# Optimization experiments

Hardware: AMD Instinct MI355X
Metric: run time of the kernel (lower is better)

The kernel has to match this reference:

```python
import jax, jax.numpy as jnp
import numpy as np

B, T, C, H, D = 2048, 64, 64, 8, 64  # batch, block_size, n_embed, num_heads, head_size


def setup_inputs() -> dict:
    key = jax.random.key(0)
    ks = jax.random.split(key, 6)
    s = C ** -0.5  # approx torch Linear init scale
    x = jax.random.normal(ks[0], (B, T, C), dtype=jnp.float32)
    Wq = jax.random.uniform(ks[1], (H, C, D), jnp.float32, -s, s)  # per-head query weights (in, out)
    Wk = jax.random.uniform(ks[2], (H, C, D), jnp.float32, -s, s)
    Wv = jax.random.uniform(ks[3], (H, C, D), jnp.float32, -s, s)
    sp = (H * D) ** -0.5
    Wproj = jax.random.uniform(ks[4], (H * D, C), jnp.float32, -sp, sp)  # proj weight (in, out)
    bproj = jax.random.uniform(ks[5], (C,), jnp.float32, -sp, sp)
    return {"x": x, "Wq": Wq, "Wk": Wk, "Wv": Wv, "Wproj": Wproj, "bproj": bproj}


def reference(x, Wq, Wk, Wv, Wproj, bproj):
    # per-head projections, vectorized over heads (original loops over Head modules)
    q = jnp.einsum('btc,hcd->bhtd', x, Wq)
    k = jnp.einsum('btc,hcd->bhtd', x, Wk)
    v = jnp.einsum('btc,hcd->bhtd', x, Wv)
    scores = jnp.einsum('bhtd,bhsd->bhts', q, k) * (D ** -0.5)  # [B,H,T,T]
    causal = jnp.tril(jnp.ones((T, T), dtype=bool))
    scores = jnp.where(causal, scores, jnp.float32(-jnp.inf))
    wei = jax.nn.softmax(scores, axis=-1)  # dropout = identity in eval mode
    out = jnp.einsum('bhts,bhsd->bhtd', wei, v)
    out = out.transpose(0, 2, 1, 3).reshape(B, T, H * D)  # concat heads on last dim
    out = out @ Wproj + bproj  # output projection (dropout = identity in eval)
    return out
```

## Files before the change

kernel.cpp:

```cpp
#include <hip/hip_runtime.h>

typedef __bf16 bf16x8 __attribute__((ext_vector_type(8)));
typedef float f32x4 __attribute__((ext_vector_type(4)));
typedef unsigned short u16x4 __attribute__((ext_vector_type(4)));
typedef unsigned int u32x4 __attribute__((ext_vector_type(4)));

#define LDA 72

template <int N> struct Int { static constexpr int value = N; };

__device__ __forceinline__ unsigned short f2bf(float f) {
  __bf16 b = (__bf16)f;
  return __builtin_bit_cast(unsigned short, b);
}

__device__ __forceinline__ u16x4 pack4(f32x4 v) {
  u16x4 r;
  r[0] = f2bf(v[0]); r[1] = f2bf(v[1]); r[2] = f2bf(v[2]); r[3] = f2bf(v[3]);
  return r;
}

__device__ __forceinline__ bf16x8 frag8(const unsigned short* p) {
  typedef unsigned short u16x8v __attribute__((ext_vector_type(8)));
  return __builtin_bit_cast(bf16x8, *reinterpret_cast<const u16x8v*>(p));
}

#define MFMA(a, b, c) __builtin_amdgcn_mfma_f32_16x16x32_bf16(a, b, c, 0, 0, 0)

__device__ __forceinline__ void cfrag2bfrag(const f32x4 v[4], bf16x8 out[2]) {
  unsigned O[4][2];
  #pragma unroll
  for (int si = 0; si < 4; ++si) {
    u16x4 p = pack4(v[si]);
    O[si][0] = (unsigned)p[0] | ((unsigned)p[1] << 16);
    O[si][1] = (unsigned)p[2] | ((unsigned)p[3] << 16);
  }
  unsigned H[2][2][2];
  #pragma unroll
  for (int s1 = 0; s1 < 2; ++s1)
    #pragma unroll
    for (int d = 0; d < 2; ++d) {
      auto r = __builtin_amdgcn_permlane32_swap(O[2 * s1][d], O[2 * s1 + 1][d], false, false);
      H[s1][0][d] = r[0];
      H[s1][1][d] = r[1];
    }
  #pragma unroll
  for (int e1 = 0; e1 < 2; ++e1) {
    auto r0 = __builtin_amdgcn_permlane16_swap(H[e1][0][0], H[e1][1][0], false, false);
    auto r1 = __builtin_amdgcn_permlane16_swap(H[e1][0][1], H[e1][1][1], false, false);
    u32x4 f;
    f[0] = r0[0]; f[1] = r1[0]; f[2] = r0[1]; f[3] = r1[1];
    out[e1] = __builtin_bit_cast(bf16x8, f);
  }
}

__global__ __launch_bounds__(256) void fuse_pack(
    const float* __restrict__ Wq, const float* __restrict__ Wk,
    const float* __restrict__ Wv, const float* __restrict__ Wp,
    unsigned short* __restrict__ wf) {
  __shared__ float A[64 * 65];
  __shared__ float B[64 * 65];
  const int blk = blockIdx.x;
  const int t = blk >> 3, h = blk & 7;
  const int tid = threadIdx.x;
  const float* Asrc = (t ? Wv : Wq) + h * 4096;
  const float* Bsrc = (t ? Wp : Wk) + h * 4096;
  for (int i = tid; i < 4096; i += 256) {
    A[(i >> 6) * 65 + (i & 63)] = Asrc[i];
    B[(i >> 6) * 65 + (i & 63)] = Bsrc[i];
  }
  __syncthreads();
  unsigned short* dst = wf + blk * 4096;
  for (int o = 0; o < 16; ++o) {
    int idx = o * 256 + tid;
    int k = idx >> 6, n = idx & 63;
    float s = 0.f;
    if (t == 0) {
      for (int d = 0; d < 64; ++d) s += A[k * 65 + d] * B[n * 65 + d];
      s *= 0.18033688f;
    } else {
      for (int d = 0; d < 64; ++d) s += A[k * 65 + d] * B[d * 65 + n];
    }
    int kk = k >> 5, i = k & 7, lg = (k >> 3) & 3, si = n >> 4, l15 = n & 15;
    dst[((kk * 4 + si) * 64 + lg * 16 + l15) * 8 + i] = f2bf(s);
  }
}

__global__ __launch_bounds__(256, 4) void mha_fwd(
    const float* __restrict__ x, const unsigned short* __restrict__ wf,
    const float* __restrict__ bproj, float* __restrict__ out) {
  __shared__ __attribute__((aligned(16))) unsigned short Xs[2][64 * LDA];

  const int tid  = threadIdx.x;
  const int lane = tid & 63;
  const int w    = tid >> 6;
  const int bt   = w >> 1;
  const int mg   = w & 1;
  const int l15  = lane & 15;
  const int g    = lane >> 4;
  const int kcol = 8 * g;

  const float* xb = x + (size_t)blockIdx.x * 8192;
  #pragma unroll
  for (int it = 0; it < 8; ++it) {
    int idx = it * 1024 + tid * 4;
    float4 v = *reinterpret_cast<const float4*>(xb + idx);
    f32x4 vv = {v.x, v.y, v.z, v.w};
    int sb = idx >> 12, rem = idx & 4095;
    *reinterpret_cast<u16x4*>(&Xs[sb][(rem >> 6) * LDA + (rem & 63)]) = pack4(vv);
  }
  __syncthreads();

  bf16x8 xf[2][4];
  #pragma unroll
  for (int cc = 0; cc < 2; ++cc)
    #pragma unroll
    for (int t = 0; t < 4; ++t)
      xf[cc][t] = frag8(&Xs[bt][(t * 16 + l15) * LDA + cc * 32 + kcol]);

  f32x4 oacc[2][4];
  #pragma unroll
  for (int nt = 0; nt < 4; ++nt) {
    float bias = bproj[nt * 16 + l15];
    f32x4 bv = {bias, bias, bias, bias};
    oacc[0][nt] = bv;
    oacc[1][nt] = bv;
  }

  #pragma unroll 1
  for (int h = 0; h < 8; ++h) {
    const unsigned short* mf = wf + h * 4096;
    const unsigned short* nf = wf + 32768 + h * 4096;

    auto head_body = [&](auto MT0C, auto MT1C) {
      constexpr int MT0 = decltype(MT0C)::value;
      constexpr int MT1 = decltype(MT1C)::value;
      bf16x8 pA[2][2];

      auto gs = [&](auto MTC, int lmt) {
        constexpr int MT = decltype(MTC)::value;
        f32x4 gc[4] = {};
        #pragma unroll
        for (int kk = 0; kk < 2; ++kk)
          #pragma unroll
          for (int ct = 0; ct < 4; ++ct)
            gc[ct] = MFMA(frag8(&mf[(kk * 4 + ct) * 512 + lane * 8]), xf[kk][MT], gc[ct]);
        bf16x8 gB[2];
        cfrag2bfrag(gc, gB);

        f32x4 sc[4] = {};
        #pragma unroll
        for (int cc = 0; cc < 2; ++cc)
          #pragma unroll
          for (int st = 0; st < 4; ++st)
            if (st <= MT)
              sc[st] = MFMA(xf[cc][st], gB[cc], sc[st]);

        const int m = MT * 16 + l15;
        float sum = 0.f;
        #pragma unroll
        for (int st = 0; st < 4; ++st) {
          if (st < MT) {
            #pragma unroll
            for (int r = 0; r < 4; ++r) { float e = exp2f(sc[st][r]); sc[st][r] = e; sum += e; }
          } else if (st == MT) {
            #pragma unroll
            for (int r = 0; r < 4; ++r) {
              int s = st * 16 + 4 * g + r;
              float e = (s <= m) ? exp2f(sc[st][r]) : 0.f;
              sc[st][r] = e; sum += e;
            }
          }
        }
        sum += __shfl_xor(sum, 16);
        sum += __shfl_xor(sum, 32);
        float rinv = __builtin_amdgcn_rcpf(sum);
        #pragma unroll
        for (int st = 0; st < 4; ++st)
          if (st <= MT) sc[st] *= rinv;
        bf16x8 o2[2];
        cfrag2bfrag(sc, o2);
        pA[0][lmt] = o2[0]; pA[1][lmt] = o2[1];
      };
      gs(Int<MT0>{}, 0);
      gs(Int<MT1>{}, 1);

      #pragma unroll
      for (int nt = 0; nt < 4; ++nt) {
        bf16x8 nf0 = frag8(&nf[nt * 512 + lane * 8]);
        bf16x8 nf1 = frag8(&nf[(4 + nt) * 512 + lane * 8]);
        f32x4 zc[4] = {};
        #pragma unroll
        for (int st = 0; st < 4; ++st) {
          zc[st] = MFMA(xf[0][st], nf0, zc[st]);
          zc[st] = MFMA(xf[1][st], nf1, zc[st]);
        }
        bf16x8 zB[2];
        cfrag2bfrag(zc, zB);
        oacc[0][nt] = MFMA(pA[0][0], zB[0], oacc[0][nt]);
        if (MT0 >= 2) oacc[0][nt] = MFMA(pA[1][0], zB[1], oacc[0][nt]);
        oacc[1][nt] = MFMA(pA[0][1], zB[0], oacc[1][nt]);
        if (MT1 >= 2) oacc[1][nt] = MFMA(pA[1][1], zB[1], oacc[1][nt]);
      }
    };

    if (mg == 0) head_body(Int<0>{}, Int<3>{});
    else         head_body(Int<1>{}, Int<2>{});
  }

  const int mtv0 = mg ? 1 : 0;
  const int mtv1 = mg ? 2 : 3;
  float* ob = out + ((size_t)blockIdx.x * 2 + bt) * 4096;
  #pragma unroll
  for (int lmt = 0; lmt < 2; ++lmt) {
    int mt = lmt ? mtv1 : mtv0;
    #pragma unroll
    for (int r = 0; r < 4; ++r) {
      float* orow = ob + (mt * 16 + 4 * g + r) * 64;
      #pragma unroll
      for (int nt = 0; nt < 4; ++nt)
        orow[nt * 16 + l15] = oacc[lmt][nt][r];
    }
  }
}

extern "C" void kernel_launch(void* const* d_in, const int* in_sizes, int n_in,
                              void* d_out, int out_size, void* d_ws, size_t ws_size,
                              hipStream_t stream) {
  const float* x  = (const float*)d_in[0];
  const float* Wq = (const float*)d_in[1];
  const float* Wk = (const float*)d_in[2];
  const float* Wv = (const float*)d_in[3];
  const float* Wp = (const float*)d_in[4];
  const float* bp = (const float*)d_in[5];
  unsigned short* wf = (unsigned short*)d_ws;

  fuse_pack<<<dim3(16), dim3(256), 0, stream>>>(Wq, Wk, Wv, Wp, wf);
  mha_fwd<<<dim3(1024), dim3(256), 0, stream>>>(x, wf, bp, (float*)d_out);
}
```

Measured before the change: 61.28 us.

## Reassociate output path to compute (P·X)·Wvp instead of P·(X·Wvp)

The value/output path is reordered. The attention probabilities are first multiplied with a transposed bf16 copy of X kept in shared memory, and the result is then multiplied by the fused Wv·Wproj weights, instead of projecting all of X per head and then applying P. This cuts the MFMA count per head and the number of fragment layout conversions, and it uses the causal structure of each row tile. The cost is a second transposed LDS buffer, which doubles shared memory per block and can limit occupancy. It also adds scalar 16-bit transposed stores during staging, which may hit bank conflicts, and the fused weight fragments are reloaded once per row tile.

```diff
diff --git a/kernel.cpp b/kernel.cpp
--- a/kernel.cpp
+++ b/kernel.cpp
@@ -90,6 +90,7 @@
     const float* __restrict__ x, const unsigned short* __restrict__ wf,
     const float* __restrict__ bproj, float* __restrict__ out) {
   __shared__ __attribute__((aligned(16))) unsigned short Xs[2][64 * LDA];
+  __shared__ __attribute__((aligned(16))) unsigned short XsT[2][64 * LDA];
 
   const int tid  = threadIdx.x;
   const int lane = tid & 63;
@@ -107,7 +108,12 @@
     float4 v = *reinterpret_cast<const float4*>(xb + idx);
     f32x4 vv = {v.x, v.y, v.z, v.w};
     int sb = idx >> 12, rem = idx & 4095;
-    *reinterpret_cast<u16x4*>(&Xs[sb][(rem >> 6) * LDA + (rem & 63)]) = pack4(vv);
+    int r = rem >> 6, c0 = rem & 63;
+    u16x4 pk = pack4(vv);
+    *reinterpret_cast<u16x4*>(&Xs[sb][r * LDA + c0]) = pk;
+    #pragma unroll
+    for (int j = 0; j < 4; ++j)
+      XsT[sb][(c0 + j) * LDA + r] = pk[j];
   }
   __syncthreads();
 
@@ -185,23 +191,28 @@
       gs(Int<MT0>{}, 0);
       gs(Int<MT1>{}, 1);
 
-      #pragma unroll
-      for (int nt = 0; nt < 4; ++nt) {
-        bf16x8 nf0 = frag8(&nf[nt * 512 + lane * 8]);
-        bf16x8 nf1 = frag8(&nf[(4 + nt) * 512 + lane * 8]);
-        f32x4 zc[4] = {};
-        #pragma unroll
-        for (int st = 0; st < 4; ++st) {
-          zc[st] = MFMA(xf[0][st], nf0, zc[st]);
-          zc[st] = MFMA(xf[1][st], nf1, zc[st]);
+      auto ypv = [&](auto MTC, int lmt) {
+        constexpr int MT = decltype(MTC)::value;
+        f32x4 ytc[4] = {};
+        #pragma unroll
+        for (int ct = 0; ct < 4; ++ct) {
+          bf16x8 xb0 = frag8(&XsT[bt][(ct * 16 + l15) * LDA + kcol]);
+          ytc[ct] = MFMA(xb0, pA[0][lmt], ytc[ct]);
+          if (MT >= 2) {
+            bf16x8 xb1 = frag8(&XsT[bt][(ct * 16 + l15) * LDA + 32 + kcol]);
+            ytc[ct] = MFMA(xb1, pA[1][lmt], ytc[ct]);
+          }
         }
-        bf16x8 zB[2];
-        cfrag2bfrag(zc, zB);
-        oacc[0][nt] = MFMA(pA[0][0], zB[0], oacc[0][nt]);
-        if (MT0 >= 2) oacc[0][nt] = MFMA(pA[1][0], zB[1], oacc[0][nt]);
-        oacc[1][nt] = MFMA(pA[0][1], zB[0], oacc[1][nt]);
-        if (MT1 >= 2) oacc[1][nt] = MFMA(pA[1][1], zB[1], oacc[1][nt]);
-      }
+        bf16x8 yA[2];
+        cfrag2bfrag(ytc, yA);
+        #pragma unroll
+        for (int nt = 0; nt < 4; ++nt) {
+          oacc[lmt][nt] = MFMA(yA[0], frag8(&nf[nt * 512 + lane * 8]), oacc[lmt][nt]);
+          oacc[lmt][nt] = MFMA(yA[1], frag8(&nf[(4 + nt) * 512 + lane * 8]), oacc[lmt][nt]);
+        }
+      };
+      ypv(Int<MT0>{}, 0);
+      ypv(Int<MT1>{}, 1);
     };
 
     if (mg == 0) head_body(Int<0>{}, Int<3>{});
```

New measurement: 63.84 us. 1.04x slower.

## Split per-head Z projection across wave pair and share via LDS

Applied to the files above, without the earlier changes.

Before, both waves covering the same batch element computed the full x·(Wv·Wproj) product for every head, so that work was done twice. Now each wave computes half of the output column tiles, writes the bf16 fragments to shared memory, and after a barrier both waves read the full set. This halves the Z-projection MFMA work in exchange for LDS traffic and one block-wide barrier per head. The Z buffers are double-buffered by head parity, and the shared memory holding the staged x is reused for them after an extra barrier.

```diff
diff --git a/kernel.cpp b/kernel.cpp
--- a/kernel.cpp
+++ b/kernel.cpp
@@ -3,6 +3,7 @@
 typedef __bf16 bf16x8 __attribute__((ext_vector_type(8)));
 typedef float f32x4 __attribute__((ext_vector_type(4)));
 typedef unsigned short u16x4 __attribute__((ext_vector_type(4)));
+typedef unsigned short u16x8 __attribute__((ext_vector_type(8)));
 typedef unsigned int u32x4 __attribute__((ext_vector_type(4)));
 
 #define LDA 72
@@ -21,8 +22,7 @@
 }
 
 __device__ __forceinline__ bf16x8 frag8(const unsigned short* p) {
-  typedef unsigned short u16x8v __attribute__((ext_vector_type(8)));
-  return __builtin_bit_cast(bf16x8, *reinterpret_cast<const u16x8v*>(p));
+  return __builtin_bit_cast(bf16x8, *reinterpret_cast<const u16x8*>(p));
 }
 
 #define MFMA(a, b, c) __builtin_amdgcn_mfma_f32_16x16x32_bf16(a, b, c, 0, 0, 0)
@@ -89,7 +89,9 @@
 __global__ __launch_bounds__(256, 4) void mha_fwd(
     const float* __restrict__ x, const unsigned short* __restrict__ wf,
     const float* __restrict__ bproj, float* __restrict__ out) {
-  __shared__ __attribute__((aligned(16))) unsigned short Xs[2][64 * LDA];
+  __shared__ __attribute__((aligned(16))) unsigned char smem[32768];
+  unsigned short* XsBase = reinterpret_cast<unsigned short*>(smem);
+  unsigned short* ZsBase = reinterpret_cast<unsigned short*>(smem);
 
   const int tid  = threadIdx.x;
   const int lane = tid & 63;
@@ -107,7 +109,7 @@
     float4 v = *reinterpret_cast<const float4*>(xb + idx);
     f32x4 vv = {v.x, v.y, v.z, v.w};
     int sb = idx >> 12, rem = idx & 4095;
-    *reinterpret_cast<u16x4*>(&Xs[sb][(rem >> 6) * LDA + (rem & 63)]) = pack4(vv);
+    *reinterpret_cast<u16x4*>(&XsBase[sb * (64 * LDA) + (rem >> 6) * LDA + (rem & 63)]) = pack4(vv);
   }
   __syncthreads();
 
@@ -116,7 +118,8 @@
   for (int cc = 0; cc < 2; ++cc)
     #pragma unroll
     for (int t = 0; t < 4; ++t)
-      xf[cc][t] = frag8(&Xs[bt][(t * 16 + l15) * LDA + cc * 32 + kcol]);
+      xf[cc][t] = frag8(&XsBase[bt * (64 * LDA) + (t * 16 + l15) * LDA + cc * 32 + kcol]);
+  __syncthreads();
 
   f32x4 oacc[2][4];
   #pragma unroll
@@ -131,12 +134,32 @@
   for (int h = 0; h < 8; ++h) {
     const unsigned short* mf = wf + h * 4096;
     const unsigned short* nf = wf + 32768 + h * 4096;
+    unsigned short* zs = ZsBase + ((bt * 2 + (h & 1)) * 8) * 64 * 8;
 
     auto head_body = [&](auto MT0C, auto MT1C) {
       constexpr int MT0 = decltype(MT0C)::value;
       constexpr int MT1 = decltype(MT1C)::value;
+
+      #pragma unroll
+      for (int l = 0; l < 2; ++l) {
+        const int ntg = 2 * mg + l;
+        bf16x8 nf0 = frag8(&nf[ntg * 512 + lane * 8]);
+        bf16x8 nf1 = frag8(&nf[(4 + ntg) * 512 + lane * 8]);
+        f32x4 zc[4] = {};
+        #pragma unroll
+        for (int st = 0; st < 4; ++st) {
+          zc[st] = MFMA(xf[0][st], nf0, zc[st]);
+          zc[st] = MFMA(xf[1][st], nf1, zc[st]);
+        }
+        bf16x8 zb[2];
+        cfrag2bfrag(zc, zb);
+        #pragma unroll
+        for (int cc = 0; cc < 2; ++cc)
+          *reinterpret_cast<u16x8*>(&zs[((ntg * 2 + cc) * 64 + lane) * 8]) =
+              __builtin_bit_cast(u16x8, zb[cc]);
+      }
+
       bf16x8 pA[2][2];
-
       auto gs = [&](auto MTC, int lmt) {
         constexpr int MT = decltype(MTC)::value;
         f32x4 gc[4] = {};
@@ -185,22 +208,16 @@
       gs(Int<MT0>{}, 0);
       gs(Int<MT1>{}, 1);
 
+      __syncthreads();
+
       #pragma unroll
       for (int nt = 0; nt < 4; ++nt) {
-        bf16x8 nf0 = frag8(&nf[nt * 512 + lane * 8]);
-        bf16x8 nf1 = frag8(&nf[(4 + nt) * 512 + lane * 8]);
-        f32x4 zc[4] = {};
-        #pragma unroll
-        for (int st = 0; st < 4; ++st) {
-          zc[st] = MFMA(xf[0][st], nf0, zc[st]);
-          zc[st] = MFMA(xf[1][st], nf1, zc[st]);
-        }
-        bf16x8 zB[2];
-        cfrag2bfrag(zc, zB);
-        oacc[0][nt] = MFMA(pA[0][0], zB[0], oacc[0][nt]);
-        if (MT0 >= 2) oacc[0][nt] = MFMA(pA[1][0], zB[1], oacc[0][nt]);
-        oacc[1][nt] = MFMA(pA[0][1], zB[0], oacc[1][nt]);
-        if (MT1 >= 2) oacc[1][nt] = MFMA(pA[1][1], zB[1], oacc[1][nt]);
+        bf16x8 zb0 = frag8(&zs[((nt * 2 + 0) * 64 + lane) * 8]);
+        oacc[0][nt] = MFMA(pA[0][0], zb0, oacc[0][nt]);
+        oacc[1][nt] = MFMA(pA[0][1], zb0, oacc[1][nt]);
+        bf16x8 zb1 = frag8(&zs[((nt * 2 + 1) * 64 + lane) * 8]);
+        if (MT0 >= 2) oacc[0][nt] = MFMA(pA[1][0], zb1, oacc[0][nt]);
+        if (MT1 >= 2) oacc[1][nt] = MFMA(pA[1][1], zb1, oacc[1][nt]);
       }
     };
 
```

After: 58.52 us. 1.05x faster.
